# Optimization experiments

Measured on AMD Instinct MI355X. Metric: run time of the kernel, lower is better.

## Reference

```python
import jax, jax.numpy as jnp
import numpy as np

B, D, H = 4096, 256, 1024
TRACE_STEPS = 10
T_FINAL = 1.0


def setup_inputs() -> dict:
    key = jax.random.key(0)
    k0, k1, k2 = jax.random.split(key, 3)
    s1 = 1.0 / np.sqrt(D + 1)
    s2 = 1.0 / np.sqrt(H)
    return {
        "x": jax.random.normal(k0, (B, D), dtype=jnp.float32),
        "W1": jax.random.uniform(k1, (D + 1, H), jnp.float32, -s1, s1),
        "b1": jnp.zeros((H,), jnp.float32),
        "W2": jax.random.uniform(k2, (H, D), jnp.float32, -s2, s2),
        "b2": jnp.zeros((D,), jnp.float32),
    }


def _odefun(params, t, z):
    # FFJORD vector field: tanh MLP on [z, t]. z: [B, D] -> [B, D]
    W1, b1, W2, b2 = params
    tcol = jnp.full((z.shape[0], 1), t, dtype=z.dtype)
    h = jnp.tanh(jnp.concatenate([z, tcol], axis=-1) @ W1 + b1)
    return h @ W2 + b2


def _rademacher(key, shape, dtype):
    # randint(0,2)*2-1, matching the torch probe construction
    return jax.random.randint(key, shape, 0, 2).astype(dtype) * 2.0 - 1.0


def _aug_dynamics(params, t, state, e):
    # state: [B, D+1] = [z | logp]; e: [TRACE_STEPS, B, D] Rademacher probes.
    # torch computes etf = grad((f*e).sum(), z) = e^T J, div = (e^T J)*e summed.
    # e^T J e == e . (J e), so forward-mode jvp gives identical math.
    z = state[:, :-1]
    f = lambda zz: _odefun(params, t, zz)

    def probe(ei):
        f_z, Je = jax.jvp(f, (z,), (ei,))
        return f_z, jnp.sum(Je * ei, axis=-1)  # [B]

    f_z, divs = jax.vmap(probe)(e)
    f_z = f_z[0]                       # primal identical across probes
    div_est = jnp.mean(divs, axis=0)   # average of trace_steps estimates
    return jnp.concatenate([f_z, -div_est[:, None]], axis=-1)


def reference(x, W1, b1, W2, b2):
    params = (W1, b1, W2, b2)
    Bx = x.shape[0]
    ekey = jax.random.key(42)
    probes = lambda i: _rademacher(jax.random.fold_in(ekey, i), (TRACE_STEPS, Bx, D), x.dtype)

    # initial augmented state: [z, logp=0]
    y0 = jnp.concatenate([x, jnp.zeros((Bx, 1), x.dtype)], axis=-1)

    # t_grid = [0, T] with 2 points -> fixed-grid rk4 takes ONE RK4 step of size T
    h = T_FINAL
    g = lambda t, y, i: _aug_dynamics(params, t, y, probes(i))
    k1 = g(0.0, y0, 0)
    k2 = g(0.5 * h, y0 + 0.5 * h * k1, 1)
    k3 = g(0.5 * h, y0 + 0.5 * h * k2, 2)
    k4 = g(h, y0 + h * k3, 3)
    y1 = y0 + (h / 6.0) * (k1 + 2.0 * k2 + 2.0 * k3 + k4)

    # module returns the full trajectory `output`: [len(t_grid), B, D+1]
    return jnp.stack([y0, y1], axis=0)
```

## Files before the change

### kernel.cpp

```cpp
#include <hip/hip_runtime.h>
#include <stdint.h>

#define BATCH 4096
#define DIMD  256
#define DIMH  1024
#define NEEL  10485760
#define NSLOT 1310720

typedef __attribute__((ext_vector_type(8))) short short8;
typedef __attribute__((ext_vector_type(4))) float float4v;

struct Keys4 { uint32_t a[4]; uint32_t b[4]; };

__host__ __device__ static inline uint32_t rotl32(uint32_t v, int r) {
#ifdef __HIP_DEVICE_COMPILE__
    return __builtin_amdgcn_alignbit(v, v, 32 - r);
#else
    return (v << r) | (v >> (32 - r));
#endif
}

__host__ __device__ static inline void tf2x32(uint32_t k0, uint32_t k1,
                                              uint32_t c0, uint32_t c1,
                                              uint32_t& o0, uint32_t& o1) {
    uint32_t ks0 = k0, ks1 = k1, ks2 = k0 ^ k1 ^ 0x1BD11BDAu;
    uint32_t x0 = c0 + ks0, x1 = c1 + ks1;
#define TF_R4(a, b, c, d)                                   \
    x0 += x1; x1 = rotl32(x1, a); x1 ^= x0;                 \
    x0 += x1; x1 = rotl32(x1, b); x1 ^= x0;                 \
    x0 += x1; x1 = rotl32(x1, c); x1 ^= x0;                 \
    x0 += x1; x1 = rotl32(x1, d); x1 ^= x0;
    TF_R4(13, 15, 26, 6)  x0 += ks1; x1 += ks2 + 1u;
    TF_R4(17, 29, 16, 24) x0 += ks2; x1 += ks0 + 2u;
    TF_R4(13, 15, 26, 6)  x0 += ks0; x1 += ks1 + 3u;
    TF_R4(17, 29, 16, 24) x0 += ks1; x1 += ks2 + 4u;
    TF_R4(13, 15, 26, 6)  x0 += ks2; x1 += ks0 + 5u;
#undef TF_R4
    o0 = x0; o1 = x1;
}

__device__ static inline short f2bf(float f) {
    uint32_t u = __float_as_uint(f);
    uint32_t r = (u + 0x7FFFu + ((u >> 16) & 1u)) >> 16;
    return (short)r;
}

__device__ static inline void egen_slot(short* __restrict__ EF, uint32_t q,
                                        uint32_t k0, uint32_t k1) {
    const uint32_t lane = q & 63u;
    const uint32_t ks   = (q >> 6) & 7u;
    const uint32_t T    = (q >> 9) & 255u;
    const uint32_t probe = q >> 17;
    const uint32_t b = T * 16u + (lane & 15u);
    const uint32_t d0 = ks * 32u + (lane >> 4) * 8u;
    const uint32_t jbase = (probe * 4096u + b) * 256u + d0;
    short8 val;
#pragma unroll
    for (int jj = 0; jj < 8; ++jj) {
        uint32_t y0, y1;
        tf2x32(k0, k1, 0u, jbase + (uint32_t)jj, y0, y1);
        val[jj] = ((y0 ^ y1) & 1u) ? (short)0x3F80 : (short)0xBF80u;
    }
    *(short8*)&EF[(size_t)q * 8] = val;
}

__global__ __launch_bounds__(256) void k_prep(
    const float* __restrict__ x,  const float* __restrict__ W1,
    const float* __restrict__ W2, short* __restrict__ W1T,
    short* __restrict__ W2B, short* __restrict__ W2T,
    short* __restrict__ zb, float* __restrict__ dv,
    short* __restrict__ E0, uint32_t ek0, uint32_t ek1)
{
    const int idx = blockIdx.x * 256 + threadIdx.x;
    if (idx < 262144) {
        const int n = idx >> 8, d = idx & 255;
        W1T[idx] = f2bf(W1[d * DIMH + n]);
    } else if (idx < 524288) {
        const int i = idx - 262144;
        W2B[i] = f2bf(W2[i]);
    } else if (idx < 786432) {
        const int i = idx - 524288;
        const int d = i >> 10, k = i & 1023;
        W2T[i] = f2bf(W2[k * DIMD + d]);
    } else if (idx < 1835008) {
        const int i = idx - 786432;
        zb[i] = f2bf(x[i]);
    } else if (idx < 1851392) {
        dv[idx - 1835008] = 0.0f;
    } else {
        egen_slot(E0, (uint32_t)(idx - 1851392), ek0, ek1);
    }
}

__global__ __launch_bounds__(256) void k_pre_div(
    const short* __restrict__ Zb, const short* __restrict__ W1T,
    const short* __restrict__ W2B, const float* __restrict__ W1,
    const float* __restrict__ b1, float tval,
    const short* __restrict__ Ecur, short* __restrict__ h_bf,
    float* __restrict__ divacc,
    short* __restrict__ Enext, uint32_t nk0, uint32_t nk1, int do_egen)
{
    __shared__ short8 Es[2048];
    const int t = threadIdx.x;
    const int b0 = blockIdx.x * 64;
    const int nt = blockIdx.y;
    const int wave = t >> 6, lane = t & 63;
    const int col = lane & 15, kq = lane >> 4;
    const int n = nt * 64 + wave * 16 + col;

    short8 bufr[8], bvfr[8];
#pragma unroll
    for (int ks = 0; ks < 8; ++ks) {
        bufr[ks] = *(const short8*)&W1T[n * DIMD + ks * 32 + kq * 8];
        bvfr[ks] = *(const short8*)&W2B[n * DIMD + ks * 32 + kq * 8];
    }

    float sreg[4][4];
    const float add = tval * W1[DIMD * DIMH + n] + b1[n];
#pragma unroll
    for (int ms = 0; ms < 4; ++ms) {
        float4v acc = {0.f, 0.f, 0.f, 0.f};
#pragma unroll
        for (int ks = 0; ks < 8; ++ks) {
            short8 af = *(const short8*)&Zb[(b0 + ms * 16 + col) * DIMD + ks * 32 + kq * 8];
            acc = __builtin_amdgcn_mfma_f32_16x16x32_bf16(af, bufr[ks], acc, 0, 0, 0);
        }
#pragma unroll
        for (int r = 0; r < 4; ++r) {
            float hv = tanhf(acc[r] + add);
            h_bf[(b0 + ms * 16 + kq * 4 + r) * DIMH + n] = f2bf(hv);
            sreg[ms][r] = 1.0f - hv * hv;
        }
    }

    float rowacc[4][4];
#pragma unroll
    for (int a = 0; a < 4; ++a)
#pragma unroll
        for (int r = 0; r < 4; ++r) rowacc[a][r] = 0.0f;

    const uint32_t bflat = (uint32_t)(blockIdx.y * 64 + blockIdx.x);
    const uint32_t qbase = bflat * 256u + (uint32_t)t;

    const int Tb = b0 >> 4;

#pragma unroll 1
    for (int probe = 0; probe < 10; ++probe) {
        if (do_egen && (probe & 1) == 0) {
            egen_slot(Enext, qbase + (uint32_t)(probe >> 1) * 262144u, nk0, nk1);
        }
        const short8* src = (const short8*)Ecur + (size_t)(probe * 256 + Tb) * 512;
        __syncthreads();
#pragma unroll
        for (int k = 0; k < 8; ++k)
            Es[t + k * 256] = src[t + k * 256];
        __syncthreads();

#pragma unroll
        for (int ms = 0; ms < 4; ++ms) {
            float4v u = {0.f, 0.f, 0.f, 0.f}, v = {0.f, 0.f, 0.f, 0.f};
#pragma unroll
            for (int ks = 0; ks < 8; ++ks) {
                short8 af = Es[((ms * 8 + ks) << 6) + lane];
                u = __builtin_amdgcn_mfma_f32_16x16x32_bf16(af, bufr[ks], u, 0, 0, 0);
                v = __builtin_amdgcn_mfma_f32_16x16x32_bf16(af, bvfr[ks], v, 0, 0, 0);
            }
#pragma unroll
            for (int r = 0; r < 4; ++r)
                rowacc[ms][r] += u[r] * sreg[ms][r] * v[r];
        }
    }

#pragma unroll
    for (int ms = 0; ms < 4; ++ms) {
#pragma unroll
        for (int r = 0; r < 4; ++r) {
            float p = rowacc[ms][r];
            p += __shfl_xor(p, 1, 64);
            p += __shfl_xor(p, 2, 64);
            p += __shfl_xor(p, 4, 64);
            p += __shfl_xor(p, 8, 64);
            rowacc[ms][r] = p;
        }
    }
    if (col == 0) {
#pragma unroll
        for (int ms = 0; ms < 4; ++ms)
#pragma unroll
            for (int r = 0; r < 4; ++r)
                atomicAdd(&divacc[b0 + ms * 16 + kq * 4 + r], rowacc[ms][r] * 0.1f);
    }
}

__global__ __launch_bounds__(256) void k_fz2(
    const short* __restrict__ Hb, const short* __restrict__ W2T,
    const float* __restrict__ b2, const float* __restrict__ x,
    float* __restrict__ rksum, float cw, int first,
    float cnext, int write_zb, short* __restrict__ zb)
{
    const int t = threadIdx.x;
    const int wave = t >> 6, lane = t & 63;
    const int col = lane & 15, kq = lane >> 4;
    const int m0 = blockIdx.x * 16;
    const int n0 = wave * 64;

    float4v acc[4];
#pragma unroll
    for (int ns = 0; ns < 4; ++ns) acc[ns] = (float4v){0.f, 0.f, 0.f, 0.f};

    const short* ap = &Hb[(m0 + col) * DIMH + kq * 8];
    short8 a_cur = *(const short8*)ap;
    short8 b_cur[4];
#pragma unroll
    for (int ns = 0; ns < 4; ++ns)
        b_cur[ns] = *(const short8*)&W2T[(n0 + ns * 16 + col) * DIMH + kq * 8];

    for (int ks = 0; ks < 31; ++ks) {
        short8 a_nxt = *(const short8*)&ap[(ks + 1) * 32];
        short8 b_nxt[4];
#pragma unroll
        for (int ns = 0; ns < 4; ++ns)
            b_nxt[ns] = *(const short8*)&W2T[(n0 + ns * 16 + col) * DIMH + (ks + 1) * 32 + kq * 8];
#pragma unroll
        for (int ns = 0; ns < 4; ++ns)
            acc[ns] = __builtin_amdgcn_mfma_f32_16x16x32_bf16(a_cur, b_cur[ns], acc[ns], 0, 0, 0);
        a_cur = a_nxt;
#pragma unroll
        for (int ns = 0; ns < 4; ++ns) b_cur[ns] = b_nxt[ns];
    }
#pragma unroll
    for (int ns = 0; ns < 4; ++ns)
        acc[ns] = __builtin_amdgcn_mfma_f32_16x16x32_bf16(a_cur, b_cur[ns], acc[ns], 0, 0, 0);

#pragma unroll
    for (int ns = 0; ns < 4; ++ns) {
        const int n = n0 + ns * 16 + col;
        const float bias = b2[n];
#pragma unroll
        for (int r = 0; r < 4; ++r) {
            const int m = m0 + kq * 4 + r;
            const int o = m * DIMD + n;
            const float val = acc[ns][r] + bias;
            const float contrib = cw * val;
            rksum[o] = first ? contrib : (rksum[o] + contrib);
            if (write_zb)
                zb[o] = f2bf(x[o] + cnext * val);
        }
    }
}

__global__ __launch_bounds__(256) void k_out(
    const float* __restrict__ x, const float* __restrict__ rksum,
    const float* __restrict__ divacc, float* __restrict__ out)
{
    const int idx = blockIdx.x * 256 + threadIdx.x;
    const int TOT = BATCH * (DIMD + 1);
    if (idx >= TOT) return;
    const int b = idx / (DIMD + 1);
    const int c = idx - b * (DIMD + 1);
    const float sixth = 1.0f / 6.0f;
    if (c < DIMD) {
        float xv = x[b * DIMD + c];
        out[idx] = xv;
        out[TOT + idx] = xv + rksum[b * DIMD + c] * sixth;
    } else {
        float d1 = divacc[b];
        float d2 = divacc[BATCH + b];
        float d3 = divacc[2 * BATCH + b];
        float d4 = divacc[3 * BATCH + b];
        out[idx] = 0.0f;
        out[TOT + idx] = -(d1 + 2.0f * d2 + 2.0f * d3 + d4) * sixth;
    }
}

extern "C" void kernel_launch(void* const* d_in, const int* in_sizes, int n_in,
                              void* d_out, int out_size, void* d_ws, size_t ws_size,
                              hipStream_t stream) {
    const float* x  = (const float*)d_in[0];
    const float* W1 = (const float*)d_in[1];
    const float* b1 = (const float*)d_in[2];
    const float* W2 = (const float*)d_in[3];
    const float* b2 = (const float*)d_in[4];
    float* out = (float*)d_out;

    char* ws = (char*)d_ws;
    short* hb    = (short*)(ws);
    float* rksum = (float*)(ws + 8388608);
    short* zb    = (short*)(ws + 12582912);
    short* w1t   = (short*)(ws + 14680064);
    short* w2b   = (short*)(ws + 15204352);
    short* w2t   = (short*)(ws + 15728640);
    float* dv    = (float*)(ws + 16252928);
    short* e0    = (short*)(ws + 16318464);
    short* e1    = (short*)(ws + 37289984);

    Keys4 keys;
    for (uint32_t i = 0; i < 4; ++i) {
        uint32_t f0, f1, g0, g1;
        tf2x32(0u, 42u, 0u, i, f0, f1);
        tf2x32(f0, f1, 0u, 1u, g0, g1);
        keys.a[i] = g0;
        keys.b[i] = g1;
    }

    k_prep<<<12352, 256, 0, stream>>>(x, W1, W2, w1t, w2b, w2t, zb, dv,
                                      e0, keys.a[0], keys.b[0]);

    const float tvals[4] = {0.0f, 0.5f, 0.5f, 1.0f};
    const float cnext[4] = {0.5f, 0.5f, 1.0f, 0.0f};
    const float cw[4]    = {1.0f, 2.0f, 2.0f, 1.0f};
    for (int s = 0; s < 4; ++s) {
        const int last = (s == 3);
        short* ecur = (s & 1) ? e1 : e0;
        short* enxt = (s & 1) ? e0 : e1;
        k_pre_div<<<dim3(64, 16), 256, 0, stream>>>(
            zb, w1t, w2b, W1, b1, tvals[s], ecur,
            hb, dv + (size_t)s * BATCH,
            enxt, last ? 0u : keys.a[s + 1], last ? 0u : keys.b[s + 1],
            last ? 0 : 1);
        k_fz2<<<256, 256, 0, stream>>>(hb, w2t, b2, x, rksum,
                                       cw[s], (s == 0) ? 1 : 0,
                                       cnext[s], (s < 3) ? 1 : 0, zb);
    }
    int tot = BATCH * (DIMD + 1);
    k_out<<<(tot + 255) / 256, 256, 0, stream>>>(x, rksum, dv, out);
}
```

Before: 496.7 us.

## Fuse output assembly into final fz2 step and stage two probes per sync

Removes the separate k_out kernel by having the last k_fz2 launch write both trajectory rows and the log-density column directly. In k_pre_div, the probe loop now loads two probes into shared memory per barrier pair (LDS doubled to 64KB) and generates the next-stage probes once per iteration. This cuts one kernel launch, an rksum round trip, and half the barriers, at the cost of higher LDS use per block, which may lower occupancy.

```diff
diff --git a/kernel.cpp b/kernel.cpp
--- a/kernel.cpp
+++ b/kernel.cpp
@@ -100,7 +100,7 @@
     float* __restrict__ divacc,
     short* __restrict__ Enext, uint32_t nk0, uint32_t nk1, int do_egen)
 {
-    __shared__ short8 Es[2048];
+    __shared__ short8 Es[4096];
     const int t = threadIdx.x;
     const int b0 = blockIdx.x * 64;
     const int nt = blockIdx.y;
@@ -145,29 +145,36 @@
     const int Tb = b0 >> 4;
 
 #pragma unroll 1
-    for (int probe = 0; probe < 10; ++probe) {
-        if (do_egen && (probe & 1) == 0) {
-            egen_slot(Enext, qbase + (uint32_t)(probe >> 1) * 262144u, nk0, nk1);
-        }
-        const short8* src = (const short8*)Ecur + (size_t)(probe * 256 + Tb) * 512;
+    for (int pp = 0; pp < 5; ++pp) {
+        if (do_egen) {
+            egen_slot(Enext, qbase + (uint32_t)pp * 262144u, nk0, nk1);
+        }
+        const short8* src0 = (const short8*)Ecur + (size_t)((2 * pp) * 256 + Tb) * 512;
+        const short8* src1 = src0 + (size_t)256 * 512;
         __syncthreads();
 #pragma unroll
         for (int k = 0; k < 8; ++k)
-            Es[t + k * 256] = src[t + k * 256];
+            Es[t + k * 256] = src0[t + k * 256];
+#pragma unroll
+        for (int k = 0; k < 8; ++k)
+            Es[2048 + t + k * 256] = src1[t + k * 256];
         __syncthreads();
 
 #pragma unroll
-        for (int ms = 0; ms < 4; ++ms) {
-            float4v u = {0.f, 0.f, 0.f, 0.f}, v = {0.f, 0.f, 0.f, 0.f};
-#pragma unroll
-            for (int ks = 0; ks < 8; ++ks) {
-                short8 af = Es[((ms * 8 + ks) << 6) + lane];
-                u = __builtin_amdgcn_mfma_f32_16x16x32_bf16(af, bufr[ks], u, 0, 0, 0);
-                v = __builtin_amdgcn_mfma_f32_16x16x32_bf16(af, bvfr[ks], v, 0, 0, 0);
+        for (int half = 0; half < 2; ++half) {
+#pragma unroll
+            for (int ms = 0; ms < 4; ++ms) {
+                float4v u = {0.f, 0.f, 0.f, 0.f}, v = {0.f, 0.f, 0.f, 0.f};
+#pragma unroll
+                for (int ks = 0; ks < 8; ++ks) {
+                    short8 af = Es[half * 2048 + ((ms * 8 + ks) << 6) + lane];
+                    u = __builtin_amdgcn_mfma_f32_16x16x32_bf16(af, bufr[ks], u, 0, 0, 0);
+                    v = __builtin_amdgcn_mfma_f32_16x16x32_bf16(af, bvfr[ks], v, 0, 0, 0);
+                }
+#pragma unroll
+                for (int r = 0; r < 4; ++r)
+                    rowacc[ms][r] += u[r] * sreg[ms][r] * v[r];
             }
-#pragma unroll
-            for (int r = 0; r < 4; ++r)
-                rowacc[ms][r] += u[r] * sreg[ms][r] * v[r];
         }
     }
 
@@ -196,13 +203,16 @@
     const short* __restrict__ Hb, const short* __restrict__ W2T,
     const float* __restrict__ b2, const float* __restrict__ x,
     float* __restrict__ rksum, float cw, int first,
-    float cnext, int write_zb, short* __restrict__ zb)
+    float cnext, int write_zb, short* __restrict__ zb,
+    int final_out, const float* __restrict__ dv, float* __restrict__ out)
 {
     const int t = threadIdx.x;
     const int wave = t >> 6, lane = t & 63;
     const int col = lane & 15, kq = lane >> 4;
     const int m0 = blockIdx.x * 16;
     const int n0 = wave * 64;
+    const int TOT = BATCH * (DIMD + 1);
+    const float sixth = 1.0f / 6.0f;
 
     float4v acc[4];
 #pragma unroll
@@ -241,35 +251,32 @@
             const int m = m0 + kq * 4 + r;
             const int o = m * DIMD + n;
             const float val = acc[ns][r] + bias;
-            const float contrib = cw * val;
-            rksum[o] = first ? contrib : (rksum[o] + contrib);
-            if (write_zb)
-                zb[o] = f2bf(x[o] + cnext * val);
-        }
-    }
-}
-
-__global__ __launch_bounds__(256) void k_out(
-    const float* __restrict__ x, const float* __restrict__ rksum,
-    const float* __restrict__ divacc, float* __restrict__ out)
-{
-    const int idx = blockIdx.x * 256 + threadIdx.x;
-    const int TOT = BATCH * (DIMD + 1);
-    if (idx >= TOT) return;
-    const int b = idx / (DIMD + 1);
-    const int c = idx - b * (DIMD + 1);
-    const float sixth = 1.0f / 6.0f;
-    if (c < DIMD) {
-        float xv = x[b * DIMD + c];
-        out[idx] = xv;
-        out[TOT + idx] = xv + rksum[b * DIMD + c] * sixth;
-    } else {
-        float d1 = divacc[b];
-        float d2 = divacc[BATCH + b];
-        float d3 = divacc[2 * BATCH + b];
-        float d4 = divacc[3 * BATCH + b];
-        out[idx] = 0.0f;
-        out[TOT + idx] = -(d1 + 2.0f * d2 + 2.0f * d3 + d4) * sixth;
+            if (final_out) {
+                const float xv = x[o];
+                out[m * (DIMD + 1) + n] = xv;
+                out[TOT + m * (DIMD + 1) + n] =
+                    xv + (rksum[o] + val) * sixth;
+            } else {
+                const float contrib = cw * val;
+                rksum[o] = first ? contrib : (rksum[o] + contrib);
+                if (write_zb)
+                    zb[o] = f2bf(x[o] + cnext * val);
+            }
+        }
+    }
+
+    if (final_out && wave == 3 && col == 0) {
+#pragma unroll
+        for (int r = 0; r < 4; ++r) {
+            const int m = m0 + kq * 4 + r;
+            const float d1 = dv[m];
+            const float d2 = dv[BATCH + m];
+            const float d3 = dv[2 * BATCH + m];
+            const float d4 = dv[3 * BATCH + m];
+            out[m * (DIMD + 1) + DIMD] = 0.0f;
+            out[TOT + m * (DIMD + 1) + DIMD] =
+                -(d1 + 2.0f * d2 + 2.0f * d3 + d4) * sixth;
+        }
     }
 }
 
@@ -320,8 +327,7 @@
             last ? 0 : 1);
         k_fz2<<<256, 256, 0, stream>>>(hb, w2t, b2, x, rksum,
                                        cw[s], (s == 0) ? 1 : 0,
-                                       cnext[s], (s < 3) ? 1 : 0, zb);
-    }
-    int tot = BATCH * (DIMD + 1);
-    k_out<<<(tot + 255) / 256, 256, 0, stream>>>(x, rksum, dv, out);
-}
+                                       cnext[s], (s < 3) ? 1 : 0, zb,
+                                       last ? 1 : 0, dv, out);
+    }
+}
```

Result: faster. 483.0 us (-2.8%).
